# Kernel tuning notes

Hardware: AMD Instinct MI355X
Metric: run time of the kernel (lower is better)

Reference implementation:

```python
import jax, jax.numpy as jnp
import numpy as np

OUT_FEATURES = 12288
IN_FEATURES = 8192
GROUP_SIZE = 64
N_GROUPS = IN_FEATURES // GROUP_SIZE      # 128
N_GROUP_IDS = GROUP_SIZE // 4             # 16 packed uint16 words per group
BATCH, SEQ = 4, 128


def _dequant(w_packed, w_scale, w_bias):
    """Unpack int4 nibbles and rescale: faithful to group_quantize_decompress.

    Packing layout (from _int4_npy_encoder): over the flattened quantized
    tensor, blocks of 16 values map to 4 packed words; value at position
    4*i + j within a block is nibble i of packed word j. The original
    decoder's float16 bit tricks ((bits & 0xF) viewed as fp16 * 2^24, etc.)
    are exactly nibble extraction.
    """
    R, G, I = w_packed.shape
    p = w_packed.reshape(R, G, I // 4, 4)                 # (R, G, blk, j)
    nibs = jnp.stack([(p >> (4 * i)) & 0xF for i in range(4)], axis=-2)  # (R, G, blk, i, j)
    unpacked = nibs.reshape(R, G, I * 4).astype(w_scale.dtype)
    w = unpacked * w_scale + w_bias                        # group scale/bias broadcast
    return w.reshape(R, G * I * 4)                         # (out_features, in_features)


def setup_inputs() -> dict:
    key = jax.random.key(0)
    k1, k2, k3, k4 = jax.random.split(key, 4)
    x = jax.random.normal(k1, (BATCH, SEQ, IN_FEATURES), dtype=jnp.float32)
    w_packed = jax.random.randint(k2, (OUT_FEATURES, N_GROUPS, N_GROUP_IDS), 0, 65536, dtype=jnp.int32)
    w_scale = jax.random.uniform(k3, (OUT_FEATURES, N_GROUPS, 1), dtype=jnp.float32) * 0.1
    w_bias = jax.random.normal(k4, (OUT_FEATURES, N_GROUPS, 1), dtype=jnp.float32) * 0.05
    return {"x": x, "w_packed": w_packed, "w_scale": w_scale, "w_bias": w_bias}


def reference(x, w_packed, w_scale, w_bias):
    weight = _dequant(w_packed, w_scale, w_bias)           # (O, I)
    return jnp.einsum('bsi,oi->bso', x, weight)            # F.linear, bias=None
```

## Files before the change

### kernel.cpp

```cpp
#include <hip/hip_runtime.h>
#include <hip/hip_bf16.h>

#define OUTF 12288
#define INF  8192
#define MTOT 512

#define BM 128
#define BN 64
#define BK 64
#define NKT 128

typedef _Float16 h2 __attribute__((ext_vector_type(2)));
typedef _Float16 h8 __attribute__((ext_vector_type(8)));
typedef float    f4 __attribute__((ext_vector_type(4)));

union U2 { unsigned int u; h2 h; };

__global__ __launch_bounds__(256) void xconvert(const float* __restrict__ x,
                                                _Float16* __restrict__ xh)
{
    int t = blockIdx.x * 256 + threadIdx.x;
    const float4* src = (const float4*)(x + (size_t)t * 16);
    float4 a = src[0];
    float4 b = src[1];
    float4 c = src[2];
    float4 d = src[3];
    U2 o0, o1, o2, o3, o4, o5, o6, o7;
    o0.h = h2{(_Float16)a.x, (_Float16)c.x};
    o1.h = h2{(_Float16)a.y, (_Float16)c.y};
    o2.h = h2{(_Float16)a.z, (_Float16)c.z};
    o3.h = h2{(_Float16)a.w, (_Float16)c.w};
    o4.h = h2{(_Float16)b.x, (_Float16)d.x};
    o5.h = h2{(_Float16)b.y, (_Float16)d.y};
    o6.h = h2{(_Float16)b.z, (_Float16)d.z};
    o7.h = h2{(_Float16)b.w, (_Float16)d.w};
    uint4* dst = (uint4*)(xh + (size_t)t * 16);
    dst[0] = make_uint4(o0.u, o1.u, o2.u, o3.u);
    dst[1] = make_uint4(o4.u, o5.u, o6.u, o7.u);
}

__global__ __launch_bounds__(256, 3) void gql_mfma(
    const _Float16* __restrict__ xh,
    const int*      __restrict__ wp,
    const float*    __restrict__ wsc,
    const float*    __restrict__ wbi,
    float*          __restrict__ out)
{
    __shared__ __align__(16) unsigned char ldsA[2][BM * BK * 2];
    __shared__ __align__(16) unsigned char ldsB[2][BN * BK * 2];

    const int tid  = threadIdx.x;
    const int lane = tid & 63;
    const int wv   = tid >> 6;
    const int wr   = wv >> 1;
    const int wc   = wv & 1;

    const int swz = (blockIdx.x & 7) * 96 + (blockIdx.x >> 3);
    const int m0  = (swz & 3) * BM;
    const int n0  = (swz >> 2) * BN;

    const _Float16* asrc[4];
#pragma unroll
    for (int ia = 0; ia < 4; ++ia) {
        int L    = ia * 4096 + tid * 16;
        int row  = L >> 7;
        int ksrc = (L & 127) ^ ((row & 7) << 4);
        asrc[ia] = xh + (size_t)(m0 + row) * INF + (ksrc >> 1);
    }

    const int brow = tid >> 2;
    const int bblk = tid & 3;
    const size_t wpo = (size_t)(n0 + brow) * 2048 + bblk * 4;
    const int sco = (n0 + brow) * 128;
    const int bw0 = brow * 128 + ((bblk * 32) ^ ((brow & 7) << 4));

    int aoff[2][4], boff[2][2];
#pragma unroll
    for (int kk = 0; kk < 2; ++kk) {
        int kb = kk * 64 + ((lane >> 4) << 4);
#pragma unroll
        for (int i = 0; i < 4; ++i) {
            int row = wr * 64 + i * 16 + (lane & 15);
            aoff[kk][i] = row * 128 + (kb ^ ((row & 7) << 4));
        }
#pragma unroll
        for (int j = 0; j < 2; ++j) {
            int col = wc * 32 + j * 16 + (lane & 15);
            boff[kk][j] = col * 128 + (kb ^ ((col & 7) << 4));
        }
    }

    f4 acc[4][2];
#pragma unroll
    for (int i = 0; i < 4; ++i)
#pragma unroll
        for (int j = 0; j < 2; ++j)
            acc[i][j] = f4{0.f, 0.f, 0.f, 0.f};

    uint4 w0, w1; float s0, s1, b0, b1;

    auto stageA = [&](int kt, int buf) {
#pragma unroll
        for (int ia = 0; ia < 4; ++ia)
            __builtin_amdgcn_global_load_lds(
                (const __attribute__((address_space(1))) void*)(asrc[ia] + kt * 64),
                (__attribute__((address_space(3))) void*)(&ldsA[buf][ia * 4096 + tid * 16]),
                16, 0, 0);
        __builtin_amdgcn_sched_barrier(0);
    };

    auto loadB = [&](int kt, uint4& w, float& s, float& b) {
        w = *(const uint4*)(wp + wpo + (size_t)kt * 16);
        s = wsc[sco + kt];
        b = wbi[sco + kt];
    };

    auto dequant = [&](uint4 w, float s, float b, int buf) {
        _Float16 sh = (_Float16)(s * 4096.0f);
        _Float16 bh = (_Float16)b;
        h2 S  = h2{sh, sh};
        h2 Bv = h2{bh, bh};
        h2 K  = h2{(_Float16)4096.0f, (_Float16)4096.0f};
        unsigned int wa[4] = {w.x, w.y, w.z, w.w};
        unsigned int ow[8];
#pragma unroll
        for (int j = 0; j < 4; ++j) {
            unsigned int t2 = wa[j] | (wa[j] << 8);
            U2 c02, c13, r02, r13;
            c02.u = t2 & 0x000F000Fu;
            c13.u = (t2 >> 4) & 0x000F000Fu;
            r02.h = (c02.h * K) * S + Bv;
            r13.h = (c13.h * K) * S + Bv;
            ow[j]     = r02.u;
            ow[4 + j] = r13.u;
        }
        *(uint4*)(&ldsB[buf][bw0])      = make_uint4(ow[0], ow[1], ow[2], ow[3]);
        *(uint4*)(&ldsB[buf][bw0 ^ 16]) = make_uint4(ow[4], ow[5], ow[6], ow[7]);
    };

    auto compute = [&](int buf) {
#pragma unroll
        for (int kk = 0; kk < 2; ++kk) {
            h8 af[4], bf[2];
#pragma unroll
            for (int i = 0; i < 4; ++i) af[i] = *(const h8*)(&ldsA[buf][aoff[kk][i]]);
#pragma unroll
            for (int j = 0; j < 2; ++j) bf[j] = *(const h8*)(&ldsB[buf][boff[kk][j]]);
#pragma unroll
            for (int i = 0; i < 4; ++i)
#pragma unroll
                for (int j = 0; j < 2; ++j)
                    acc[i][j] = __builtin_amdgcn_mfma_f32_16x16x32_f16(af[i], bf[j], acc[i][j], 0, 0, 0);
        }
    };

#define KBAR(n) do { asm volatile("s_waitcnt vmcnt(" #n ") lgkmcnt(0)" ::: "memory"); \
                     __builtin_amdgcn_s_barrier(); } while (0)

    stageA(0, 0);
    loadB(0, w0, s0, b0);
    loadB(1, w1, s1, b1);
    dequant(w0, s0, b0, 0);
    KBAR(3);

    for (int kt = 0; kt < NKT - 2; kt += 2) {
        stageA(kt + 1, 1);
        loadB(kt + 2, w0, s0, b0);
        compute(0);
        dequant(w1, s1, b1, 1);
        KBAR(3);

        stageA(kt + 2, 0);
        loadB(kt + 3, w1, s1, b1);
        compute(1);
        dequant(w0, s0, b0, 0);
        KBAR(3);
    }
    stageA(NKT - 1, 1);
    compute(0);
    dequant(w1, s1, b1, 1);
    KBAR(0);
    compute(1);

    const int cr = (lane >> 4) << 2;
    const int cc = lane & 15;
#pragma unroll
    for (int i = 0; i < 4; ++i)
#pragma unroll
        for (int j = 0; j < 2; ++j) {
            int grow = m0 + wr * 64 + i * 16 + cr;
            int gcol = n0 + wc * 32 + j * 16 + cc;
            float* p = out + (size_t)grow * OUTF + gcol;
            p[0 * OUTF] = acc[i][j][0];
            p[1 * OUTF] = acc[i][j][1];
            p[2 * OUTF] = acc[i][j][2];
            p[3 * OUTF] = acc[i][j][3];
        }
#undef KBAR
}

extern "C" void kernel_launch(void* const* d_in, const int* in_sizes, int n_in,
                              void* d_out, int out_size, void* d_ws, size_t ws_size,
                              hipStream_t stream)
{
    const float* x  = (const float*)d_in[0];
    const int*   wq = (const int*)d_in[1];
    const float* ws = (const float*)d_in[2];
    const float* wb = (const float*)d_in[3];
    float* o        = (float*)d_out;
    _Float16* xh    = (_Float16*)d_ws;

    xconvert<<<(MTOT * (size_t)INF / 16) / 256, 256, 0, stream>>>(x, xh);
    gql_mfma<<<(MTOT / BM) * (OUTF / BN), 256, 0, stream>>>(xh, wq, ws, wb, o);
}
```

Measured before the change: 312.2 us.

## Widen N tile to 96 with six waves and register-staged A loads

Raises the output tile width from 64 to 96 columns and the block size from 256 to 384 threads (six waves in a 2x3 grid). This cuts the grid to 512 blocks and remaps blocks so each XCD handles one M tile and half of N. The A tile now goes through registers with a two-deep buffer in place of direct global-to-LDS loads, and the vmcnt waits are gone. Each block reuses more of its A tile, at the cost of extra registers, extra LDS writes from threads, and a possible lower occupancy at 384 threads.

```diff
diff --git a/kernel.cpp b/kernel.cpp
--- a/kernel.cpp
+++ b/kernel.cpp
@@ -6,7 +6,7 @@
 #define MTOT 512
 
 #define BM 128
-#define BN 64
+#define BN 96
 #define BK 64
 #define NKT 128
 
@@ -39,7 +39,7 @@
     dst[1] = make_uint4(o4.u, o5.u, o6.u, o7.u);
 }
 
-__global__ __launch_bounds__(256, 3) void gql_mfma(
+__global__ __launch_bounds__(384, 3) void gql_mfma(
     const _Float16* __restrict__ xh,
     const int*      __restrict__ wp,
     const float*    __restrict__ wsc,
@@ -52,20 +52,23 @@
     const int tid  = threadIdx.x;
     const int lane = tid & 63;
     const int wv   = tid >> 6;
-    const int wr   = wv >> 1;
-    const int wc   = wv & 1;
-
-    const int swz = (blockIdx.x & 7) * 96 + (blockIdx.x >> 3);
-    const int m0  = (swz & 3) * BM;
-    const int n0  = (swz >> 2) * BN;
-
-    const _Float16* asrc[4];
-#pragma unroll
-    for (int ia = 0; ia < 4; ++ia) {
-        int L    = ia * 4096 + tid * 16;
+    const int wr   = (wv >= 3) ? 1 : 0;
+    const int wc   = wv - wr * 3;
+
+    const int xcd = blockIdx.x & 7;
+    const int jt  = blockIdx.x >> 3;
+    const int m0  = (xcd >> 1) * BM;
+    const int n0  = ((xcd & 1) * 64 + jt) * BN;
+
+    const _Float16* asrc[3];
+    int aldsoff[3];
+#pragma unroll
+    for (int c = 0; c < 3; ++c) {
+        int L    = (c < 2) ? (c * 6144 + tid * 16) : (12288 + tid * 16);
         int row  = L >> 7;
         int ksrc = (L & 127) ^ ((row & 7) << 4);
-        asrc[ia] = xh + (size_t)(m0 + row) * INF + (ksrc >> 1);
+        asrc[c]    = xh + (size_t)(m0 + row) * INF + (ksrc >> 1);
+        aldsoff[c] = L;
     }
 
     const int brow = tid >> 2;
@@ -97,18 +100,16 @@
         for (int j = 0; j < 2; ++j)
             acc[i][j] = f4{0.f, 0.f, 0.f, 0.f};
 
-    uint4 w0, w1; float s0, s1, b0, b1;
-
-    auto stageA = [&](int kt, int buf) {
-#pragma unroll
-        for (int ia = 0; ia < 4; ++ia)
-            __builtin_amdgcn_global_load_lds(
-                (const __attribute__((address_space(1))) void*)(asrc[ia] + kt * 64),
-                (__attribute__((address_space(3))) void*)(&ldsA[buf][ia * 4096 + tid * 16]),
-                16, 0, 0);
-        __builtin_amdgcn_sched_barrier(0);
-    };
-
+    auto loadA = [&](int kt, uint4* ar) {
+        ar[0] = *(const uint4*)(asrc[0] + kt * 64);
+        ar[1] = *(const uint4*)(asrc[1] + kt * 64);
+        if (tid < 256) ar[2] = *(const uint4*)(asrc[2] + kt * 64);
+    };
+    auto writeA = [&](const uint4* ar, int buf) {
+        *(uint4*)(&ldsA[buf][aldsoff[0]]) = ar[0];
+        *(uint4*)(&ldsA[buf][aldsoff[1]]) = ar[1];
+        if (tid < 256) *(uint4*)(&ldsA[buf][aldsoff[2]]) = ar[2];
+    };
     auto loadB = [&](int kt, uint4& w, float& s, float& b) {
         w = *(const uint4*)(wp + wpo + (size_t)kt * 16);
         s = wsc[sco + kt];
@@ -154,32 +155,33 @@
         }
     };
 
-#define KBAR(n) do { asm volatile("s_waitcnt vmcnt(" #n ") lgkmcnt(0)" ::: "memory"); \
-                     __builtin_amdgcn_s_barrier(); } while (0)
-
-    stageA(0, 0);
-    loadB(0, w0, s0, b0);
-    loadB(1, w1, s1, b1);
-    dequant(w0, s0, b0, 0);
-    KBAR(3);
+#define LBAR() do { asm volatile("s_waitcnt lgkmcnt(0)" ::: "memory"); \
+                    __builtin_amdgcn_s_barrier(); } while (0)
+
+    uint4 arP[3], arQ[3];
+    uint4 wwP; float sP, bP;
+    uint4 wwQ; float sQ, bQ;
+
+    loadA(0, arP); loadB(0, wwP, sP, bP);
+    writeA(arP, 0); dequant(wwP, sP, bP, 0);
+    loadA(1, arP); loadB(1, wwP, sP, bP);
+    LBAR();
 
     for (int kt = 0; kt < NKT - 2; kt += 2) {
-        stageA(kt + 1, 1);
-        loadB(kt + 2, w0, s0, b0);
+        loadA(kt + 2, arQ); loadB(kt + 2, wwQ, sQ, bQ);
+        writeA(arP, 1); dequant(wwP, sP, bP, 1);
         compute(0);
-        dequant(w1, s1, b1, 1);
-        KBAR(3);
-
-        stageA(kt + 2, 0);
-        loadB(kt + 3, w1, s1, b1);
+        LBAR();
+
+        loadA(kt + 3, arP); loadB(kt + 3, wwP, sP, bP);
+        writeA(arQ, 0); dequant(wwQ, sQ, bQ, 0);
         compute(1);
-        dequant(w0, s0, b0, 0);
-        KBAR(3);
+        LBAR();
     }
-    stageA(NKT - 1, 1);
+
+    writeA(arP, 1); dequant(wwP, sP, bP, 1);
     compute(0);
-    dequant(w1, s1, b1, 1);
-    KBAR(0);
+    LBAR();
     compute(1);
 
     const int cr = (lane >> 4) << 2;
@@ -196,7 +198,7 @@
             p[2 * OUTF] = acc[i][j][2];
             p[3 * OUTF] = acc[i][j][3];
         }
-#undef KBAR
+#undef LBAR
 }
 
 extern "C" void kernel_launch(void* const* d_in, const int* in_sizes, int n_in,
@@ -211,5 +213,5 @@
     _Float16* xh    = (_Float16*)d_ws;
 
     xconvert<<<(MTOT * (size_t)INF / 16) / 256, 256, 0, stream>>>(x, xh);
-    gql_mfma<<<(MTOT / BM) * (OUTF / BN), 256, 0, stream>>>(xh, wq, ws, wb, o);
+    gql_mfma<<<(MTOT / BM) * (OUTF / BN), 384, 0, stream>>>(xh, wq, ws, wb, o);
 }
```

Measured after the change: 463.6 us. 48.5% more time.
